# Performance work log

Hardware: AMD Instinct MI355X
Metric: run time of the kernel (lower is better)

The kernel has to match this reference:

```python
import jax, jax.numpy as jnp
import numpy as np

ALPHA = 0.1   # GCN2Conv initial-residual strength
THETA = 0.5   # GCN2Conv identity-mapping strength
NUM_LAYERS = 3
N_GRAPHS = 256


def setup_inputs() -> dict:
    key = jax.random.key(0)
    ks = jax.random.split(key, 8)
    N, E, IN, HID, OUT = 50000, 800000, 128, 64, 10
    x = jax.random.normal(ks[0], (N, IN), dtype=jnp.float32)
    edge_index = jax.random.randint(ks[1], (2, E), 0, N, dtype=jnp.int64)
    batch = jnp.sort(jax.random.randint(ks[2], (N,), 0, N_GRAPHS, dtype=jnp.int64))
    s_in = 1.0 / np.sqrt(IN)
    s_h = 1.0 / np.sqrt(HID)
    lin1_w = jax.random.uniform(ks[3], (IN, HID), jnp.float32, -s_in, s_in)
    lin1_b = jax.random.uniform(ks[4], (HID,), jnp.float32, -s_in, s_in)
    conv_ws = jax.random.uniform(ks[5], (NUM_LAYERS, HID, HID), jnp.float32, -s_h, s_h)
    lin2_w = jax.random.uniform(ks[6], (HID, OUT), jnp.float32, -s_h, s_h)
    lin2_b = jax.random.uniform(ks[7], (OUT,), jnp.float32, -s_h, s_h)
    return {"x": x, "edge_index": edge_index, "batch": batch,
            "lin1_w": lin1_w, "lin1_b": lin1_b, "conv_ws": conv_ws,
            "lin2_w": lin2_w, "lin2_b": lin2_b}


def reference(x, edge_index, batch, lin1_w, lin1_b, conv_ws, lin2_w, lin2_b):
    n = x.shape[0]
    # gcn_norm: add self-loops, symmetric deg^-1/2 normalization
    loops = jnp.arange(n, dtype=edge_index.dtype)
    row = jnp.concatenate([edge_index[0], loops])  # source nodes
    col = jnp.concatenate([edge_index[1], loops])  # target nodes
    deg = jax.ops.segment_sum(jnp.ones_like(row, dtype=x.dtype), col, num_segments=n)
    dinv = jnp.where(deg > 0, jax.lax.rsqrt(jnp.maximum(deg, 1.0)), 0.0)
    norm = dinv[row] * dinv[col]  # [E+N]

    h = jax.nn.relu(x @ lin1_w + lin1_b)  # [N, HID]
    h0 = h
    for i in range(conv_ws.shape[0]):
        beta = float(np.log(THETA / (i + 1) + 1.0))
        # sparse neighbor aggregation: gather messages, segment-sum at targets
        msgs = h[row] * norm[:, None]                     # [E+N, HID]
        agg = jax.ops.segment_sum(msgs, col, num_segments=n)
        s = (1.0 - ALPHA) * agg + ALPHA * h0              # initial residual
        h = jax.nn.relu((1.0 - beta) * s + beta * (s @ conv_ws[i]))

    # global_mean_pool over batch ids
    sums = jax.ops.segment_sum(h, batch, num_segments=N_GRAPHS)
    counts = jax.ops.segment_sum(jnp.ones((n,), x.dtype), batch, num_segments=N_GRAPHS)
    pooled = sums / jnp.maximum(counts, 1.0)[:, None]     # [N_GRAPHS, HID]
    return pooled @ lin2_w + lin2_b
```

## Files before the change

### kernel.cpp

```cpp
#include <hip/hip_runtime.h>
#include <hip/hip_fp16.h>
#include <math.h>

constexpr int IN_F = 128;
constexpr int HID  = 64;
constexpr int OUT_F = 10;
constexpr int NG   = 256;
constexpr int BSH  = 7;
constexpr int BNODES = 1 << BSH;
constexpr int CAP  = 3072;
constexpr int NBUK_MAX = 1024;
constexpr int EPB  = 8192;
constexpr int EMAX = 1024;
constexpr int NLAYER = 3;

typedef _Float16 half8 __attribute__((ext_vector_type(8)));
typedef float f32x4 __attribute__((ext_vector_type(4)));

__global__ void k_detect(const unsigned int* w, int nwords, int* flag,
                         int* gcur, int nbuk,
                         const float* __restrict__ convw,
                         unsigned short* __restrict__ w16t) {
    __shared__ int nz;
    if (threadIdx.x == 0) nz = 0;
    for (int t = threadIdx.x; t < nbuk; t += 256) gcur[t] = 0;
    for (int idx = threadIdx.x; idx < NLAYER * HID * HID; idx += 256) {
        int layer = idx >> 12;
        int rem = idx & 4095;
        int n = rem >> 6, k = rem & 63;
        w16t[idx] = __half_as_ushort(__float2half(convw[layer * 4096 + k * HID + n]));
    }
    __syncthreads();
    int seen = 0;
    for (int i = 1 + 2 * (int)threadIdx.x; i < nwords; i += 2 * (int)blockDim.x)
        if (w[i] != 0u) seen = 1;
    if (seen) atomicOr(&nz, 1);
    __syncthreads();
    if (threadIdx.x == 0) *flag = (nz == 0) ? 1 : 0;
}

__device__ __forceinline__ int ld_idx(const void* p, long long i, int is64) {
    return is64 ? (int)((const long long*)p)[i] : ((const int*)p)[i];
}

__global__ __launch_bounds__(1024) void k_bucket2(const void* eidx, const int* f64,
                                                  int E, int nbuk,
                                                  int* gcur, unsigned* bucketed) {
    __shared__ int lhist[NBUK_MAX];
    __shared__ int lofs[NBUK_MAX];
    __shared__ int lcur[NBUK_MAX];
    __shared__ unsigned stage[EPB];
    __shared__ unsigned short sbid[EPB];
    int tid = threadIdx.x;
    long long base = (long long)blockIdx.x * EPB;
    int nval = (int)min((long long)EPB, (long long)E - base);
    int is64 = *f64;
    lhist[tid] = 0; lcur[tid] = 0;
    __syncthreads();
    unsigned pv[8]; int bv[8];
    #pragma unroll
    for (int j = 0; j < 8; ++j) {
        long long e = base + j * 1024 + tid;
        if (e < E) {
            int r = ld_idx(eidx, e, is64);
            int c = ld_idx(eidx, (long long)E + e, is64);
            int b = c >> BSH;
            pv[j] = (unsigned)r | ((unsigned)(c & (BNODES - 1)) << 20);
            bv[j] = b;
            atomicAdd(&lhist[b], 1);
        } else bv[j] = -1;
    }
    __syncthreads();
    lofs[tid] = lhist[tid];
    __syncthreads();
    for (int off = 1; off < NBUK_MAX; off <<= 1) {
        int v = (tid >= off) ? lofs[tid - off] : 0;
        __syncthreads();
        lofs[tid] += v;
        __syncthreads();
    }
    int cnt = lhist[tid];
    if (tid < nbuk && cnt > 0)
        lhist[tid] = atomicAdd(&gcur[tid], cnt);
    #pragma unroll
    for (int j = 0; j < 8; ++j) {
        if (bv[j] >= 0) {
            int b = bv[j];
            int ex = (b > 0) ? lofs[b - 1] : 0;
            int p = ex + atomicAdd(&lcur[b], 1);
            stage[p] = pv[j];
            sbid[p] = (unsigned short)b;
        }
    }
    __syncthreads();
    for (int p = tid; p < nval; p += 1024) {
        int b = sbid[p];
        int ex = (b > 0) ? lofs[b - 1] : 0;
        int dst = lhist[b] + (p - ex);
        if (dst < CAP)
            bucketed[(long long)b * CAP + dst] = stage[p];
    }
}

__global__ void k_bucket_fb(const void* eidx, const int* f64, int E,
                            int* gcur, unsigned* bucketed) {
    int e = blockIdx.x * blockDim.x + threadIdx.x;
    if (e >= E) return;
    int is64 = *f64;
    int r = ld_idx(eidx, e, is64);
    int c = ld_idx(eidx, (long long)E + e, is64);
    int b = c >> BSH;
    int pos = atomicAdd(&gcur[b], 1);
    if (pos < CAP)
        bucketed[(long long)b * CAP + pos] =
            (unsigned)r | ((unsigned)(c & (BNODES - 1)) << 20);
}

__global__ __launch_bounds__(512) void k_bscan(const int* __restrict__ gcur,
                                               int* __restrict__ gofs, int nbuk,
                                               int* rowptr, int N,
                                               float* psum, float* pcnt) {
    int tid = threadIdx.x;
    for (int t = tid; t < NG * HID; t += 512) psum[t] = 0.f;
    for (int t = tid; t < NG; t += 512) pcnt[t] = 0.f;
    __shared__ int tot[512];
    int chunk = (nbuk + 511) / 512;
    int st = tid * chunk, en = min(st + chunk, nbuk);
    int s = 0;
    for (int i = st; i < en; ++i) s += min(gcur[i], CAP);
    tot[tid] = s;
    __syncthreads();
    for (int off = 1; off < 512; off <<= 1) {
        int a = (tid >= off) ? tot[tid - off] : 0;
        __syncthreads();
        tot[tid] += a;
        __syncthreads();
    }
    int run = tot[tid] - s;
    for (int i = st; i < en; ++i) { gofs[i] = run; run += min(gcur[i], CAP); }
    if (tid == 511) rowptr[N] = tot[511];
}

__global__ __launch_bounds__(256) void k_bfill(const int* __restrict__ gcur,
                                               const int* __restrict__ gofs,
                                               const unsigned* __restrict__ bucketed,
                                               int* __restrict__ rowptr,
                                               float* __restrict__ dinv,
                                               int* __restrict__ csr_src, int N) {
    __shared__ int lhist[BNODES], lrp[BNODES], lcur[BNODES];
    __shared__ int stage[CAP];
    int b = blockIdx.x;
    int cnt = min(gcur[b], CAP);
    int base = gofs[b];
    int nb0 = b << BSH;
    int tid = threadIdx.x;
    const unsigned* bk = bucketed + (long long)b * CAP;
    if (tid < BNODES) { lhist[tid] = 0; lcur[tid] = 0; }
    __syncthreads();
    for (int t = tid; t < cnt; t += 256) atomicAdd(&lhist[bk[t] >> 20], 1);
    __syncthreads();
    if (tid < BNODES) lrp[tid] = lhist[tid];
    __syncthreads();
    for (int off = 1; off < BNODES; off <<= 1) {
        int a = (tid < BNODES && tid >= off) ? lrp[tid - off] : 0;
        __syncthreads();
        if (tid < BNODES) lrp[tid] += a;
        __syncthreads();
    }
    if (tid < BNODES) {
        int ex = lrp[tid] - lhist[tid];
        lrp[tid] = ex;
        int node = nb0 + tid;
        if (node < N) {
            rowptr[node] = base + ex;
            dinv[node] = rsqrtf((float)lhist[tid] + 1.0f);
        }
    }
    __syncthreads();
    for (int t = tid; t < cnt; t += 256) {
        unsigned v = bk[t];
        int lc = v >> 20;
        int q = atomicAdd(&lcur[lc], 1);
        stage[lrp[lc] + q] = (int)(v & 0xFFFFFu);
    }
    __syncthreads();
    for (int t = tid; t < cnt; t += 256) csr_src[base + t] = stage[t];
}

constexpr int LNB = 64;
__global__ __launch_bounds__(256) void k_lin1(const float* __restrict__ x,
                                              const float* __restrict__ w1,
                                              const float* __restrict__ b1,
                                              const float* __restrict__ dinv,
                                              unsigned short* __restrict__ h0,
                                              unsigned short* __restrict__ hs0, int N) {
    __shared__ unsigned short xs[LNB][IN_F];
    __shared__ unsigned short wt[HID][IN_F];
    int tid = threadIdx.x;
    int l = tid & 63, wv = tid >> 6;
    int nb0 = blockIdx.x * LNB;

    for (int t = tid; t < (IN_F * HID / 4); t += 256) {
        int k = t >> 4;
        int n0 = (t & 15) * 4;
        float4 v = *(const float4*)&w1[k * HID + n0];
        int kc = k >> 3, ke = k & 7;
        wt[n0 + 0][((kc ^ ((n0 + 0) & 15)) * 8) + ke] = __half_as_ushort(__float2half(v.x));
        wt[n0 + 1][((kc ^ ((n0 + 1) & 15)) * 8) + ke] = __half_as_ushort(__float2half(v.y));
        wt[n0 + 2][((kc ^ ((n0 + 2) & 15)) * 8) + ke] = __half_as_ushort(__float2half(v.z));
        wt[n0 + 3][((kc ^ ((n0 + 3) & 15)) * 8) + ke] = __half_as_ushort(__float2half(v.w));
    }
    for (int t = tid; t < LNB * (IN_F / 8); t += 256) {
        int row = t >> 4, kc = t & 15;
        int gn = nb0 + row;
        float4 va = make_float4(0.f, 0.f, 0.f, 0.f), vb = va;
        if (gn < N) {
            va = ((const float4*)x)[(long long)gn * 32 + kc * 2];
            vb = ((const float4*)x)[(long long)gn * 32 + kc * 2 + 1];
        }
        __attribute__((aligned(16))) unsigned short t8[8];
        t8[0] = __half_as_ushort(__float2half(va.x));
        t8[1] = __half_as_ushort(__float2half(va.y));
        t8[2] = __half_as_ushort(__float2half(va.z));
        t8[3] = __half_as_ushort(__float2half(va.w));
        t8[4] = __half_as_ushort(__float2half(vb.x));
        t8[5] = __half_as_ushort(__float2half(vb.y));
        t8[6] = __half_as_ushort(__float2half(vb.z));
        t8[7] = __half_as_ushort(__float2half(vb.w));
        int slot = kc ^ (row & 15);
        *(uint4*)&xs[row][slot * 8] = *(uint4*)t8;
    }
    __syncthreads();

    int i16 = l & 15, hk = l >> 4;
    f32x4 acc0 = {0.f,0.f,0.f,0.f}, acc1 = acc0, acc2 = acc0, acc3 = acc0;
    #pragma unroll
    for (int kc4 = 0; kc4 < 4; ++kc4) {
        int kc = kc4 * 4 + hk;
        int arow = wv * 16 + i16;
        half8 av = *(half8*)&xs[arow][(kc ^ (arow & 15)) * 8];
        half8 b0 = *(half8*)&wt[ 0 + i16][(kc ^ (( 0 + i16) & 15)) * 8];
        half8 b1v = *(half8*)&wt[16 + i16][(kc ^ ((16 + i16) & 15)) * 8];
        half8 b2v = *(half8*)&wt[32 + i16][(kc ^ ((32 + i16) & 15)) * 8];
        half8 b3v = *(half8*)&wt[48 + i16][(kc ^ ((48 + i16) & 15)) * 8];
        acc0 = __builtin_amdgcn_mfma_f32_16x16x32_f16(av, b0,  acc0, 0, 0, 0);
        acc1 = __builtin_amdgcn_mfma_f32_16x16x32_f16(av, b1v, acc1, 0, 0, 0);
        acc2 = __builtin_amdgcn_mfma_f32_16x16x32_f16(av, b2v, acc2, 0, 0, 0);
        acc3 = __builtin_amdgcn_mfma_f32_16x16x32_f16(av, b3v, acc3, 0, 0, 0);
    }
    #pragma unroll
    for (int r = 0; r < 4; ++r) {
        int gn = nb0 + wv * 16 + hk * 4 + r;
        if (gn >= N) continue;
        float di = dinv[gn];
        float vr[4] = {acc0[r], acc1[r], acc2[r], acc3[r]};
        #pragma unroll
        for (int ct = 0; ct < 4; ++ct) {
            int col = ct * 16 + i16;
            float v = fmaxf(vr[ct] + b1[col], 0.f);
            h0 [(long long)gn * HID + col] = __half_as_ushort(__float2half(v));
            hs0[(long long)gn * HID + col] = __half_as_ushort(__float2half(v * di));
        }
    }
}

__global__ __launch_bounds__(256) void k_layer(const int* __restrict__ rowptr,
                                               const int* __restrict__ csr_src,
                                               const float* __restrict__ dinv,
                                               const unsigned short* __restrict__ hs_in,
                                               const unsigned short* __restrict__ h0,
                                               const unsigned short* __restrict__ w16,
                                               float beta, int scale_out,
                                               unsigned short* __restrict__ h_out, int N) {
    __shared__ unsigned short s_lds[16][HID];
    __shared__ unsigned short wt_lds[HID][HID];
    __shared__ int ldsidx[EMAX];
    __shared__ int lrowp[17];
    int tid = threadIdx.x;
    int l = tid & 63, wv = tid >> 6;
    int nb = blockIdx.x * 16;

    if (tid < 17) lrowp[tid] = rowptr[min(nb + tid, N)];
    #pragma unroll
    for (int uu = 0; uu < 2; ++uu) {
        int u = tid * 2 + uu;
        int n = u >> 3, kb = u & 7;
        uint4 v = ((const uint4*)w16)[u];
        *(uint4*)&wt_lds[n][(kb ^ (n & 7)) * 8] = v;
    }
    __syncthreads();

    int eblk0 = lrowp[0];
    int ecnt = lrowp[16] - eblk0;
    bool use_lds = (ecnt <= EMAX);
    if (use_lds)
        for (int t = tid; t < ecnt; t += 256) ldsidx[t] = csr_src[eblk0 + t];
    __syncthreads();

    const uint4* hin4 = (const uint4*)hs_in;
    const uint4* h04  = (const uint4*)h0;
    int j = l >> 4, q = (l >> 3) & 1, m = l & 7;
    int row = wv * 4 + j;
    int node = nb + row;
    int e0 = lrowp[row], e1 = lrowp[row + 1];

    __half2 a[4] = {__half2(0.f, 0.f), __half2(0.f, 0.f),
                    __half2(0.f, 0.f), __half2(0.f, 0.f)};
    __half2 b[4] = {__half2(0.f, 0.f), __half2(0.f, 0.f),
                    __half2(0.f, 0.f), __half2(0.f, 0.f)};
    int e = e0 + q;
    if (use_lds) {
        const int* lx = ldsidx - eblk0;
        for (; e + 6 < e1; e += 8) {
            int r0 = lx[e], r1 = lx[e + 2], r2 = lx[e + 4], r3 = lx[e + 6];
            uint4 v0 = hin4[(long long)r0 * 8 + m];
            uint4 v1 = hin4[(long long)r1 * 8 + m];
            uint4 v2 = hin4[(long long)r2 * 8 + m];
            uint4 v3 = hin4[(long long)r3 * 8 + m];
            const __half2 *p0 = (const __half2*)&v0, *p1 = (const __half2*)&v1;
            const __half2 *p2 = (const __half2*)&v2, *p3 = (const __half2*)&v3;
            #pragma unroll
            for (int jj = 0; jj < 4; ++jj) {
                a[jj] = __hadd2(a[jj], p0[jj]);
                b[jj] = __hadd2(b[jj], p1[jj]);
            }
            #pragma unroll
            for (int jj = 0; jj < 4; ++jj) {
                a[jj] = __hadd2(a[jj], p2[jj]);
                b[jj] = __hadd2(b[jj], p3[jj]);
            }
        }
        for (; e < e1; e += 2) {
            uint4 v = hin4[(long long)lx[e] * 8 + m];
            const __half2* p = (const __half2*)&v;
            #pragma unroll
            for (int jj = 0; jj < 4; ++jj) a[jj] = __hadd2(a[jj], p[jj]);
        }
    } else {
        for (; e + 6 < e1; e += 8) {
            int r0 = csr_src[e], r1 = csr_src[e + 2];
            int r2 = csr_src[e + 4], r3 = csr_src[e + 6];
            uint4 v0 = hin4[(long long)r0 * 8 + m];
            uint4 v1 = hin4[(long long)r1 * 8 + m];
            uint4 v2 = hin4[(long long)r2 * 8 + m];
            uint4 v3 = hin4[(long long)r3 * 8 + m];
            const __half2 *p0 = (const __half2*)&v0, *p1 = (const __half2*)&v1;
            const __half2 *p2 = (const __half2*)&v2, *p3 = (const __half2*)&v3;
            #pragma unroll
            for (int jj = 0; jj < 4; ++jj) {
                a[jj] = __hadd2(a[jj], p0[jj]);
                b[jj] = __hadd2(b[jj], p1[jj]);
            }
            #pragma unroll
            for (int jj = 0; jj < 4; ++jj) {
                a[jj] = __hadd2(a[jj], p2[jj]);
                b[jj] = __hadd2(b[jj], p3[jj]);
            }
        }
        for (; e < e1; e += 2) {
            uint4 v = hin4[(long long)csr_src[e] * 8 + m];
            const __half2* p = (const __half2*)&v;
            #pragma unroll
            for (int jj = 0; jj < 4; ++jj) a[jj] = __hadd2(a[jj], p[jj]);
        }
    }
    #pragma unroll
    for (int jj = 0; jj < 4; ++jj) a[jj] = __hadd2(a[jj], b[jj]);
    #pragma unroll
    for (int jj = 0; jj < 4; ++jj) {
        unsigned t = __shfl_xor(*(unsigned*)&a[jj], 8, 64);
        a[jj] = __hadd2(a[jj], *(__half2*)&t);
    }
    if (q == 0) {
        if (node < N) {
            float di = dinv[node];
            uint4 hv = hin4[(long long)node * 8 + m];
            uint4 rv = h04 [(long long)node * 8 + m];
            const __half2* hp = (const __half2*)&hv;
            const __half2* rp = (const __half2*)&rv;
            __attribute__((aligned(16))) unsigned short out8[8];
            #pragma unroll
            for (int jj = 0; jj < 4; ++jj) {
                __half2 t = __hadd2(a[jj], hp[jj]);
                float slo = fmaf(0.9f * di, __low2float(t),  0.1f * __low2float(rp[jj]));
                float shi = fmaf(0.9f * di, __high2float(t), 0.1f * __high2float(rp[jj]));
                *(__half2*)&out8[jj * 2] = __floats2half2_rn(slo, shi);
            }
            int slot = m ^ (row & 7);
            *(uint4*)&s_lds[row][slot * 8] = *(uint4*)out8;
        } else {
            int slot = m ^ (row & 7);
            uint4 z = make_uint4(0, 0, 0, 0);
            *(uint4*)&s_lds[row][slot * 8] = z;
        }
    }
    __syncthreads();

    int i16 = l & 15, kc = l >> 4;
    f32x4 acc = {0.f, 0.f, 0.f, 0.f};
    #pragma unroll
    for (int ks = 0; ks < 2; ++ks) {
        int cb = ks * 4 + kc;
        int sa = cb ^ (i16 & 7);
        half8 av = *(half8*)&s_lds[i16][sa * 8];
        int n = wv * 16 + i16;
        int sb = cb ^ (n & 7);
        half8 bv = *(half8*)&wt_lds[n][sb * 8];
        acc = __builtin_amdgcn_mfma_f32_16x16x32_f16(av, bv, acc, 0, 0, 0);
    }
    #pragma unroll
    for (int r = 0; r < 4; ++r) {
        int orow = kc * 4 + r;
        int onode = nb + orow;
        if (onode < N) {
            int colg = wv * 16 + i16;
            int slot = (colg >> 3) ^ (orow & 7);
            __half sh = *(__half*)&s_lds[orow][slot * 8 + (colg & 7)];
            float sv = __half2float(sh);
            float v = fmaxf(sv + beta * (acc[r] - sv), 0.f);
            if (scale_out) v *= dinv[onode];
            __half hv2 = __float2half(v);
            h_out[(long long)onode * HID + colg] = *(unsigned short*)&hv2;
        }
    }
}

constexpr int POOL_CHUNK = 256;
__global__ __launch_bounds__(256) void k_pool(const unsigned short* __restrict__ h,
                                              const void* batch, const int* f64,
                                              float* psum, float* pcnt, int N) {
    int c = threadIdx.x & 63;
    int g = threadIdx.x >> 6;
    int n0 = blockIdx.x * POOL_CHUNK;
    int nend = min(n0 + POOL_CHUNK, N);
    int is64 = *f64;
    float sum = 0.f;
    int cnt = 0, curb = -1;
    for (int n = n0 + g; n < nend; n += 4) {
        int b = ld_idx(batch, n, is64);
        if (b != curb) {
            if (curb >= 0) {
                atomicAdd(&psum[(long long)curb * HID + c], sum);
                if (c == 0) atomicAdd(&pcnt[curb], (float)cnt);
            }
            curb = b; sum = 0.f; cnt = 0;
        }
        __half hv = *(__half*)&h[(long long)n * HID + c];
        sum += __half2float(hv);
        cnt++;
    }
    if (curb >= 0) {
        atomicAdd(&psum[(long long)curb * HID + c], sum);
        if (c == 0) atomicAdd(&pcnt[curb], (float)cnt);
    }
}

__global__ void k_out(const float* __restrict__ psum, const float* __restrict__ pcnt,
                      const float* __restrict__ w2, const float* __restrict__ b2,
                      float* __restrict__ out) {
    int g = blockIdx.x;
    int tid = threadIdx.x;
    __shared__ float pr[HID];
    float cnt = fmaxf(pcnt[g], 1.0f);
    pr[tid] = psum[(long long)g * HID + tid] / cnt;
    __syncthreads();
    if (tid < OUT_F) {
        float acc = b2[tid];
        #pragma unroll
        for (int k = 0; k < HID; ++k)
            acc = fmaf(pr[k], w2[k * OUT_F + tid], acc);
        out[g * OUT_F + tid] = acc;
    }
}

static inline size_t align256(size_t x) { return (x + 255) & ~(size_t)255; }

extern "C" void kernel_launch(void* const* d_in, const int* in_sizes, int n_in,
                              void* d_out, int out_size, void* d_ws, size_t ws_size,
                              hipStream_t stream) {
    const float* x     = (const float*)d_in[0];
    const void*  eidx  = d_in[1];
    const void*  batch = d_in[2];
    const float* w1    = (const float*)d_in[3];
    const float* b1    = (const float*)d_in[4];
    const float* convw = (const float*)d_in[5];
    const float* w2    = (const float*)d_in[6];
    const float* b2    = (const float*)d_in[7];
    float* out = (float*)d_out;

    int N = in_sizes[0] / IN_F;
    int E = in_sizes[1] / 2;
    int nbuk = (N + BNODES - 1) >> BSH;

    char* ws = (char*)d_ws;
    float* dinv    = (float*)ws;                ws += align256((size_t)N * 4);
    unsigned short* h0  = (unsigned short*)ws;  ws += align256((size_t)N * HID * 2);
    unsigned short* hs0 = (unsigned short*)ws;  ws += align256((size_t)N * HID * 2);
    unsigned short* hb  = (unsigned short*)ws;  ws += align256((size_t)N * HID * 2);
    float* psum    = (float*)ws;                ws += align256((size_t)NG * HID * 4);
    float* pcnt    = (float*)ws;                ws += align256((size_t)NG * 4);
    int*   rowptr  = (int*)ws;                  ws += align256((size_t)(N + 1) * 4);
    int*   csr_src = (int*)ws;                  ws += align256((size_t)E * 4);
    int*   gcur    = (int*)ws;                  ws += align256((size_t)nbuk * 4);
    int*   gofs    = (int*)ws;                  ws += align256((size_t)(nbuk + 1) * 4);
    unsigned short* w16t = (unsigned short*)ws; ws += align256((size_t)NLAYER * HID * HID * 2);
    unsigned* bucketed = (unsigned*)ws;         ws += align256((size_t)nbuk * CAP * 4);
    int*   flag    = (int*)ws;

    k_detect<<<1, 256, 0, stream>>>((const unsigned int*)eidx, 4096, flag, gcur, nbuk,
                                    convw, w16t);

    if (nbuk <= NBUK_MAX)
        k_bucket2<<<(E + EPB - 1) / EPB, 1024, 0, stream>>>(eidx, flag, E, nbuk,
                                                            gcur, bucketed);
    else
        k_bucket_fb<<<(E + 255) / 256, 256, 0, stream>>>(eidx, flag, E, gcur, bucketed);
    k_bscan<<<1, 512, 0, stream>>>(gcur, gofs, nbuk, rowptr, N, psum, pcnt);
    k_bfill<<<nbuk, 256, 0, stream>>>(gcur, gofs, bucketed, rowptr, dinv, csr_src, N);

    k_lin1<<<(N + LNB - 1) / LNB, 256, 0, stream>>>(x, w1, b1, dinv, h0, hs0, N);

    int nlb = (N + 15) / 16;
    float beta0 = logf(0.5f / 1.0f + 1.0f);
    float beta1 = logf(0.5f / 2.0f + 1.0f);
    float beta2 = logf(0.5f / 3.0f + 1.0f);
    k_layer<<<nlb, 256, 0, stream>>>(rowptr, csr_src, dinv, hs0, h0,
                                     w16t + 0 * HID * HID, beta0, 1, hb, N);
    k_layer<<<nlb, 256, 0, stream>>>(rowptr, csr_src, dinv, hb, h0,
                                     w16t + 1 * HID * HID, beta1, 1, hs0, N);
    k_layer<<<nlb, 256, 0, stream>>>(rowptr, csr_src, dinv, hs0, h0,
                                     w16t + 2 * HID * HID, beta2, 0, hb, N);

    k_pool<<<(N + POOL_CHUNK - 1) / POOL_CHUNK, 256, 0, stream>>>(hb, batch, flag,
                                                                  psum, pcnt, N);
    k_out<<<NG, 64, 0, stream>>>(psum, pcnt, w2, b2, out);
}
```

Measured before the change: 135.6 us.

## Fold bucket scan into bfill and fuse output projection into pool via last-block

Removes the single-block k_bscan launch: each k_bfill block now computes its own base offset by reducing gcur over the preceding buckets, and psum/pcnt zeroing moves into k_detect. k_out is removed by having the last-finishing k_pool block (detected with an atomic counter) compute the mean-pool and lin2 projection. Pool reads are widened to half2 per lane. This cuts two kernel launches and their serialization, at the cost of redundant prefix reduction per block and a serial tail done by a single block.

Result: no change. 134.9 us (-0.5%).

```diff
diff --git a/kernel.cpp b/kernel.cpp
--- a/kernel.cpp
+++ b/kernel.cpp
@@ -20,10 +20,13 @@
 __global__ void k_detect(const unsigned int* w, int nwords, int* flag,
                          int* gcur, int nbuk,
                          const float* __restrict__ convw,
-                         unsigned short* __restrict__ w16t) {
+                         unsigned short* __restrict__ w16t,
+                         float* psum, float* pcnt, int* done) {
     __shared__ int nz;
-    if (threadIdx.x == 0) nz = 0;
+    if (threadIdx.x == 0) { nz = 0; *done = 0; }
     for (int t = threadIdx.x; t < nbuk; t += 256) gcur[t] = 0;
+    for (int t = threadIdx.x; t < NG * HID; t += 256) psum[t] = 0.f;
+    for (int t = threadIdx.x; t < NG; t += 256) pcnt[t] = 0.f;
     for (int idx = threadIdx.x; idx < NLAYER * HID * HID; idx += 256) {
         int layer = idx >> 12;
         int rem = idx & 4095;
@@ -116,45 +119,32 @@
             (unsigned)r | ((unsigned)(c & (BNODES - 1)) << 20);
 }
 
-__global__ __launch_bounds__(512) void k_bscan(const int* __restrict__ gcur,
-                                               int* __restrict__ gofs, int nbuk,
-                                               int* rowptr, int N,
-                                               float* psum, float* pcnt) {
-    int tid = threadIdx.x;
-    for (int t = tid; t < NG * HID; t += 512) psum[t] = 0.f;
-    for (int t = tid; t < NG; t += 512) pcnt[t] = 0.f;
-    __shared__ int tot[512];
-    int chunk = (nbuk + 511) / 512;
-    int st = tid * chunk, en = min(st + chunk, nbuk);
-    int s = 0;
-    for (int i = st; i < en; ++i) s += min(gcur[i], CAP);
-    tot[tid] = s;
-    __syncthreads();
-    for (int off = 1; off < 512; off <<= 1) {
-        int a = (tid >= off) ? tot[tid - off] : 0;
-        __syncthreads();
-        tot[tid] += a;
-        __syncthreads();
-    }
-    int run = tot[tid] - s;
-    for (int i = st; i < en; ++i) { gofs[i] = run; run += min(gcur[i], CAP); }
-    if (tid == 511) rowptr[N] = tot[511];
-}
-
 __global__ __launch_bounds__(256) void k_bfill(const int* __restrict__ gcur,
-                                               const int* __restrict__ gofs,
                                                const unsigned* __restrict__ bucketed,
                                                int* __restrict__ rowptr,
                                                float* __restrict__ dinv,
-                                               int* __restrict__ csr_src, int N) {
+                                               int* __restrict__ csr_src,
+                                               int N, int nbuk) {
     __shared__ int lhist[BNODES], lrp[BNODES], lcur[BNODES];
     __shared__ int stage[CAP];
     int b = blockIdx.x;
     int cnt = min(gcur[b], CAP);
-    int base = gofs[b];
     int nb0 = b << BSH;
     int tid = threadIdx.x;
     const unsigned* bk = bucketed + (long long)b * CAP;
+
+    int s = 0;
+    for (int i = tid; i < b; i += 256) s += min(gcur[i], CAP);
+    stage[tid] = s;
+    __syncthreads();
+    for (int off = 128; off > 0; off >>= 1) {
+        if (tid < off) stage[tid] += stage[tid + off];
+        __syncthreads();
+    }
+    int base = stage[0];
+    __syncthreads();
+    if (b == nbuk - 1 && tid == 0) rowptr[N] = base + cnt;
+
     if (tid < BNODES) { lhist[tid] = 0; lcur[tid] = 0; }
     __syncthreads();
     for (int t = tid; t < cnt; t += 256) atomicAdd(&lhist[bk[t] >> 20], 1);
@@ -428,48 +418,64 @@
 constexpr int POOL_CHUNK = 256;
 __global__ __launch_bounds__(256) void k_pool(const unsigned short* __restrict__ h,
                                               const void* batch, const int* f64,
-                                              float* psum, float* pcnt, int N) {
-    int c = threadIdx.x & 63;
-    int g = threadIdx.x >> 6;
+                                              float* psum, float* pcnt, int N,
+                                              const float* __restrict__ w2,
+                                              const float* __restrict__ b2,
+                                              float* __restrict__ out,
+                                              int* done, int nblocks) {
+    __shared__ int islast;
+    int tid = threadIdx.x;
+    int g = tid >> 5;
+    int lane = tid & 31;
     int n0 = blockIdx.x * POOL_CHUNK;
     int nend = min(n0 + POOL_CHUNK, N);
     int is64 = *f64;
-    float sum = 0.f;
+    const unsigned* h2 = (const unsigned*)h;
+    float sx = 0.f, sy = 0.f;
     int cnt = 0, curb = -1;
-    for (int n = n0 + g; n < nend; n += 4) {
+    for (int n = n0 + g; n < nend; n += 8) {
         int b = ld_idx(batch, n, is64);
         if (b != curb) {
             if (curb >= 0) {
-                atomicAdd(&psum[(long long)curb * HID + c], sum);
-                if (c == 0) atomicAdd(&pcnt[curb], (float)cnt);
+                atomicAdd(&psum[(long long)curb * HID + lane * 2], sx);
+                atomicAdd(&psum[(long long)curb * HID + lane * 2 + 1], sy);
+                if (lane == 0) atomicAdd(&pcnt[curb], (float)cnt);
             }
-            curb = b; sum = 0.f; cnt = 0;
-        }
-        __half hv = *(__half*)&h[(long long)n * HID + c];
-        sum += __half2float(hv);
+            curb = b; sx = 0.f; sy = 0.f; cnt = 0;
+        }
+        unsigned v = h2[(long long)n * 32 + lane];
+        __half2 hv = *(__half2*)&v;
+        sx += __low2float(hv);
+        sy += __high2float(hv);
         cnt++;
     }
     if (curb >= 0) {
-        atomicAdd(&psum[(long long)curb * HID + c], sum);
-        if (c == 0) atomicAdd(&pcnt[curb], (float)cnt);
-    }
-}
-
-__global__ void k_out(const float* __restrict__ psum, const float* __restrict__ pcnt,
-                      const float* __restrict__ w2, const float* __restrict__ b2,
-                      float* __restrict__ out) {
-    int g = blockIdx.x;
-    int tid = threadIdx.x;
-    __shared__ float pr[HID];
-    float cnt = fmaxf(pcnt[g], 1.0f);
-    pr[tid] = psum[(long long)g * HID + tid] / cnt;
-    __syncthreads();
-    if (tid < OUT_F) {
-        float acc = b2[tid];
+        atomicAdd(&psum[(long long)curb * HID + lane * 2], sx);
+        atomicAdd(&psum[(long long)curb * HID + lane * 2 + 1], sy);
+        if (lane == 0) atomicAdd(&pcnt[curb], (float)cnt);
+    }
+    __threadfence();
+    __syncthreads();
+    if (tid == 0) {
+        int v = atomicAdd(done, 1);
+        islast = (v == nblocks - 1) ? 1 : 0;
+    }
+    __syncthreads();
+    if (!islast) return;
+    __threadfence();
+    for (int gg = tid; gg < NG; gg += 256) {
+        float c = fmaxf(pcnt[gg], 1.0f);
+        float acc[OUT_F];
         #pragma unroll
-        for (int k = 0; k < HID; ++k)
-            acc = fmaf(pr[k], w2[k * OUT_F + tid], acc);
-        out[g * OUT_F + tid] = acc;
+        for (int o = 0; o < OUT_F; ++o) acc[o] = b2[o];
+        for (int k = 0; k < HID; ++k) {
+            float p = psum[(long long)gg * HID + k] / c;
+            #pragma unroll
+            for (int o = 0; o < OUT_F; ++o)
+                acc[o] = fmaf(p, w2[k * OUT_F + o], acc[o]);
+        }
+        #pragma unroll
+        for (int o = 0; o < OUT_F; ++o) out[gg * OUT_F + o] = acc[o];
     }
 }
 
@@ -502,21 +508,20 @@
     int*   rowptr  = (int*)ws;                  ws += align256((size_t)(N + 1) * 4);
     int*   csr_src = (int*)ws;                  ws += align256((size_t)E * 4);
     int*   gcur    = (int*)ws;                  ws += align256((size_t)nbuk * 4);
-    int*   gofs    = (int*)ws;                  ws += align256((size_t)(nbuk + 1) * 4);
     unsigned short* w16t = (unsigned short*)ws; ws += align256((size_t)NLAYER * HID * HID * 2);
     unsigned* bucketed = (unsigned*)ws;         ws += align256((size_t)nbuk * CAP * 4);
-    int*   flag    = (int*)ws;
+    int*   flag    = (int*)ws;                  ws += align256(4);
+    int*   done    = (int*)ws;
 
     k_detect<<<1, 256, 0, stream>>>((const unsigned int*)eidx, 4096, flag, gcur, nbuk,
-                                    convw, w16t);
+                                    convw, w16t, psum, pcnt, done);
 
     if (nbuk <= NBUK_MAX)
         k_bucket2<<<(E + EPB - 1) / EPB, 1024, 0, stream>>>(eidx, flag, E, nbuk,
                                                             gcur, bucketed);
     else
         k_bucket_fb<<<(E + 255) / 256, 256, 0, stream>>>(eidx, flag, E, gcur, bucketed);
-    k_bscan<<<1, 512, 0, stream>>>(gcur, gofs, nbuk, rowptr, N, psum, pcnt);
-    k_bfill<<<nbuk, 256, 0, stream>>>(gcur, gofs, bucketed, rowptr, dinv, csr_src, N);
+    k_bfill<<<nbuk, 256, 0, stream>>>(gcur, bucketed, rowptr, dinv, csr_src, N, nbuk);
 
     k_lin1<<<(N + LNB - 1) / LNB, 256, 0, stream>>>(x, w1, b1, dinv, h0, hs0, N);
 
@@ -531,7 +536,7 @@
     k_layer<<<nlb, 256, 0, stream>>>(rowptr, csr_src, dinv, hs0, h0,
                                      w16t + 2 * HID * HID, beta2, 0, hb, N);
 
-    k_pool<<<(N + POOL_CHUNK - 1) / POOL_CHUNK, 256, 0, stream>>>(hb, batch, flag,
-                                                                  psum, pcnt, N);
-    k_out<<<NG, 64, 0, stream>>>(psum, pcnt, w2, b2, out);
-}
+    int npb = (N + POOL_CHUNK - 1) / POOL_CHUNK;
+    k_pool<<<npb, 256, 0, stream>>>(hb, batch, flag, psum, pcnt, N,
+                                    w2, b2, out, done, npb);
+}
```
